# Optimization experiments

Measured on AMD Instinct MI355X. Metric: run time of the kernel, lower is better.

## Reference

```python
import jax, jax.numpy as jnp
import numpy as np

B, S, D, H = 2, 2048, 1024, 16
HD = D // H

def setup_inputs() -> dict:
    key = jax.random.key(0)
    k1, k2, k3, k4, k5 = jax.random.split(key, 5)
    X = jax.random.normal(k1, (B, S, D), dtype=jnp.float32)
    # nn.Linear(D, 3D): weight [3D, D], bias [3D]
    W_qkv = jax.random.normal(k2, (3 * D, D), dtype=jnp.float32) * (1.0 / np.sqrt(D))
    b_qkv = jax.random.normal(k3, (3 * D,), dtype=jnp.float32) * 0.02
    W_out = jax.random.normal(k4, (D, D), dtype=jnp.float32) * (1.0 / np.sqrt(D))
    b_out = jax.random.normal(k5, (D,), dtype=jnp.float32) * 0.02
    return {"X": X, "W_qkv": W_qkv, "b_qkv": b_qkv, "W_out": W_out, "b_out": b_out}

def reference(X, W_qkv, b_qkv, W_out, b_out):
    b, s, d = X.shape
    qkv = jnp.einsum('bsd,ed->bse', X, W_qkv) + b_qkv  # [B,S,3D]
    q, k, v = jnp.split(qkv, 3, axis=2)
    def heads(t):
        return t.reshape(b, s, H, HD).transpose(0, 2, 1, 3)  # [B,H,S,HD]
    q, k, v = heads(q), heads(k), heads(v)
    scores = jnp.einsum('bhqd,bhkd->bhqk', q, k) * (1.0 / np.sqrt(HD))
    causal = jnp.tril(jnp.ones((s, s), dtype=bool))
    scores = jnp.where(causal[None, None], scores, jnp.float32(-jnp.inf))
    probs = jax.nn.softmax(scores, axis=-1)
    attn = jnp.einsum('bhqk,bhkd->bhqd', probs, v)  # [B,H,S,HD]
    attn = attn.transpose(0, 2, 1, 3).reshape(b, s, d)
    out = jnp.einsum('bsd,ed->bse', attn, W_out) + b_out
    return out
```

## Files before the change

kernel.cpp:

```cpp
#include <hip/hip_runtime.h>


typedef _Float16 f16x8 __attribute__((ext_vector_type(8)));
typedef _Float16 f16x4 __attribute__((ext_vector_type(4)));
typedef float    f32x4 __attribute__((ext_vector_type(4)));
typedef unsigned short u16x8 __attribute__((ext_vector_type(8)));

__device__ __forceinline__ float bf16_bits_to_f32(unsigned short u) {
    union { unsigned int i; float f; } v; v.i = ((unsigned int)u) << 16; return v.f;
}
__device__ __forceinline__ unsigned short f32_to_bf16_bits(float f) {
    union { float f; unsigned int i; } v; v.f = f;
    unsigned int x = v.i;
    return (unsigned short)((x + 0x7fffu + ((x >> 16) & 1u)) >> 16);
}
__device__ __forceinline__ float fexp2(float x) {
#if __has_builtin(__builtin_amdgcn_exp2f)
    return __builtin_amdgcn_exp2f(x);
#else
    return exp2f(x);
#endif
}
__device__ __forceinline__ void gll16(const void* g, void* l) {
    __builtin_amdgcn_global_load_lds(
        (const __attribute__((address_space(1))) unsigned int*)g,
        (__attribute__((address_space(3))) unsigned int*)l, 16, 0, 0);
}

__global__ void detect_kernel(const unsigned short* __restrict__ X, unsigned int* __restrict__ flag) {
    __shared__ unsigned int smax;
    if (threadIdx.x == 0) smax = 0;
    __syncthreads();
    unsigned int mymax = 0;
    for (int i = threadIdx.x; i < 16384; i += 256) {
        unsigned int e = (X[i] >> 7) & 0xFFu;
        mymax = mymax > e ? mymax : e;
    }
    atomicMax(&smax, mymax);
    __syncthreads();
    if (threadIdx.x == 0) flag[0] = (smax >= 0x90u) ? 1u : 0u;
}

__global__ void __launch_bounds__(256) cvtw_kernel(const void* __restrict__ in,
                                                   _Float16* __restrict__ out,
                                                   const unsigned int* __restrict__ flag) {
    size_t i = ((size_t)blockIdx.x * 256 + threadIdx.x) * 8;
    f16x8 c;
    if (flag[0]) {
        const float* p = (const float*)in + i;
        #pragma unroll
        for (int j = 0; j < 8; j++) c[j] = (_Float16)p[j];
    } else {
        u16x8 r = *(const u16x8*)((const unsigned short*)in + i);
        #pragma unroll
        for (int j = 0; j < 8; j++) c[j] = (_Float16)bf16_bits_to_f32(r[j]);
    }
    *(f16x8*)(out + i) = c;
}

template<int AF16>
__global__ void __launch_bounds__(256) qkv_gemm(
    const void* __restrict__ A, const _Float16* __restrict__ Wf,
    const void* __restrict__ bias, const unsigned int* __restrict__ flag,
    _Float16* __restrict__ qws, _Float16* __restrict__ kws, _Float16* __restrict__ vtws)
{
    constexpr int AST = AF16 ? 32 : 56;
    __shared__ _Float16 As[128 * AST];
    __shared__ _Float16 Bs[128 * 32];
    const bool isf32 = (flag[0] != 0u);
    const int tid  = threadIdx.x;
    const int lane = tid & 63, wave = tid >> 6;
    const int l15  = lane & 15, quad = lane >> 4;
    const int wm   = (wave >> 1) * 64, wn = (wave & 1) * 64;
    const int m0   = blockIdx.y * 128, n0 = blockIdx.x * 128;
    const int srow = tid >> 1, scol = (tid & 1) * 16;

    f32x4 acc[4][4] = {};

    for (int k0 = 0; k0 < 1024; k0 += 32) {
        if (AF16) {
            #pragma unroll
            for (int i = 0; i < 2; i++) {
                int seg = (wave * 2 + i) * 64 + lane;
                int row = seg >> 2, qtr = seg & 3;
                gll16((const _Float16*)A + (size_t)(m0 + row) * 1024 + k0 + qtr * 8,
                      &As[(wave * 2 + i) * 512]);
            }
        } else {
            f16x8 c0, c1;
            if (isf32) {
                const float4* ga = (const float4*)((const float*)A + (size_t)(m0 + srow) * 1024 + k0 + scol);
                float4 a0 = ga[0], a1 = ga[1], a2 = ga[2], a3 = ga[3];
                c0[0]=(_Float16)a0.x; c0[1]=(_Float16)a0.y; c0[2]=(_Float16)a0.z; c0[3]=(_Float16)a0.w;
                c0[4]=(_Float16)a1.x; c0[5]=(_Float16)a1.y; c0[6]=(_Float16)a1.z; c0[7]=(_Float16)a1.w;
                c1[0]=(_Float16)a2.x; c1[1]=(_Float16)a2.y; c1[2]=(_Float16)a2.z; c1[3]=(_Float16)a2.w;
                c1[4]=(_Float16)a3.x; c1[5]=(_Float16)a3.y; c1[6]=(_Float16)a3.z; c1[7]=(_Float16)a3.w;
            } else {
                const unsigned short* ga = (const unsigned short*)A + (size_t)(m0 + srow) * 1024 + k0 + scol;
                u16x8 r0 = *(const u16x8*)ga, r1 = *(const u16x8*)(ga + 8);
                #pragma unroll
                for (int i = 0; i < 8; i++) {
                    c0[i] = (_Float16)bf16_bits_to_f32(r0[i]);
                    c1[i] = (_Float16)bf16_bits_to_f32(r1[i]);
                }
            }
            *(f16x8*)&As[srow * AST + scol]     = c0;
            *(f16x8*)&As[srow * AST + scol + 8] = c1;
        }
        #pragma unroll
        for (int i = 0; i < 2; i++) {
            int seg = (wave * 2 + i) * 64 + lane;
            int row = seg >> 2, qtr = seg & 3;
            gll16(Wf + (size_t)(n0 + row) * 1024 + k0 + qtr * 8, &Bs[(wave * 2 + i) * 512]);
        }
        __syncthreads();
        f16x8 af[4], bfg[4];
        #pragma unroll
        for (int mt = 0; mt < 4; mt++)
            af[mt] = *(const f16x8*)&As[(wm + mt * 16 + l15) * AST + quad * 8];
        #pragma unroll
        for (int nt = 0; nt < 4; nt++)
            bfg[nt] = *(const f16x8*)&Bs[(wn + nt * 16 + l15) * 32 + quad * 8];
        #pragma unroll
        for (int mt = 0; mt < 4; mt++)
            #pragma unroll
            for (int nt = 0; nt < 4; nt++)
                acc[mt][nt] = __builtin_amdgcn_mfma_f32_16x16x32_f16(af[mt], bfg[nt], acc[mt][nt], 0, 0, 0);
        __syncthreads();
    }

    #pragma unroll
    for (int mt = 0; mt < 4; mt++) {
        #pragma unroll
        for (int nt = 0; nt < 4; nt++) {
            #pragma unroll
            for (int r = 0; r < 4; r++) {
                int m = m0 + wm + mt * 16 + quad * 4 + r;
                int n = n0 + wn + nt * 16 + l15;
                float bval = isf32 ? ((const float*)bias)[n] : bf16_bits_to_f32(((const unsigned short*)bias)[n]);
                float val = acc[mt][nt][r] + bval;
                int b = m >> 11, s = m & 2047;
                int t = n >> 10, e = n & 1023;
                int h = e >> 6, hd = e & 63;
                int bh = b * 16 + h;
                if (t == 0)      qws[((size_t)bh * 2048 + s) * 64 + hd]  = (_Float16)val;
                else if (t == 1) kws[((size_t)bh * 2048 + s) * 64 + hd]  = (_Float16)val;
                else             vtws[((size_t)bh * 64 + hd) * 2048 + s] = (_Float16)val;
            }
        }
    }
}

__global__ void __launch_bounds__(256) out_gemm(
    const _Float16* __restrict__ Alo, const _Float16* __restrict__ Ahi,
    const _Float16* __restrict__ Wf, const void* __restrict__ bias,
    const unsigned int* __restrict__ flag, void* __restrict__ outp, int m_base)
{
    __shared__ _Float16 As[128 * 32];
    __shared__ _Float16 Bs[128 * 32];
    const bool isf32 = (flag[0] != 0u);
    const int tid  = threadIdx.x;
    const int lane = tid & 63, wave = tid >> 6;
    const int l15  = lane & 15, quad = lane >> 4;
    const int wm   = (wave >> 1) * 64, wn = (wave & 1) * 64;
    const int m0g  = m_base + blockIdx.y * 128, n0 = blockIdx.x * 128;
    const _Float16* A = (m0g < 2048) ? (Alo + (size_t)m0g * 1024)
                                     : (Ahi + (size_t)(m0g - 2048) * 1024);
    f32x4 acc[4][4] = {};

    for (int k0 = 0; k0 < 1024; k0 += 32) {
        #pragma unroll
        for (int i = 0; i < 2; i++) {
            int seg = (wave * 2 + i) * 64 + lane;
            int row = seg >> 2, qtr = seg & 3;
            gll16(A + (size_t)row * 1024 + k0 + qtr * 8, &As[(wave * 2 + i) * 512]);
            gll16(Wf + (size_t)(n0 + row) * 1024 + k0 + qtr * 8, &Bs[(wave * 2 + i) * 512]);
        }
        __syncthreads();
        f16x8 af[4], bfg[4];
        #pragma unroll
        for (int mt = 0; mt < 4; mt++)
            af[mt] = *(const f16x8*)&As[(wm + mt * 16 + l15) * 32 + quad * 8];
        #pragma unroll
        for (int nt = 0; nt < 4; nt++)
            bfg[nt] = *(const f16x8*)&Bs[(wn + nt * 16 + l15) * 32 + quad * 8];
        #pragma unroll
        for (int mt = 0; mt < 4; mt++)
            #pragma unroll
            for (int nt = 0; nt < 4; nt++)
                acc[mt][nt] = __builtin_amdgcn_mfma_f32_16x16x32_f16(af[mt], bfg[nt], acc[mt][nt], 0, 0, 0);
        __syncthreads();
    }

    #pragma unroll
    for (int mt = 0; mt < 4; mt++) {
        #pragma unroll
        for (int nt = 0; nt < 4; nt++) {
            #pragma unroll
            for (int r = 0; r < 4; r++) {
                int m = m0g + wm + mt * 16 + quad * 4 + r;
                int n = n0 + wn + nt * 16 + l15;
                float bval = isf32 ? ((const float*)bias)[n] : bf16_bits_to_f32(((const unsigned short*)bias)[n]);
                float val = acc[mt][nt][r] + bval;
                size_t idx = (size_t)m * 1024 + n;
                if (isf32) ((float*)outp)[idx] = val;
                else       ((unsigned short*)outp)[idx] = f32_to_bf16_bits(val);
            }
        }
    }
}

__global__ void __launch_bounds__(256) flash_kernel(
    const _Float16* __restrict__ qws,
    const _Float16* __restrict__ kws,
    const _Float16* __restrict__ vtws,
    _Float16* __restrict__ attn_lo,
    _Float16* __restrict__ attn_hi)
{
    __shared__ _Float16 Ks[2][64 * 64];
    __shared__ _Float16 Vs[2][64 * 72];

    const int bh   = blockIdx.x;
    const int qb   = 15 - blockIdx.y;
    const int Q0   = qb * 128;
    const int tid  = threadIdx.x;
    const int wave = tid >> 6;
    const int lane = tid & 63;
    const int l15  = lane & 15, quad = lane >> 4;

    const _Float16* Q  = qws  + (size_t)bh * 2048 * 64;
    const _Float16* Kp = kws  + (size_t)bh * 2048 * 64;
    const _Float16* Vt = vtws + (size_t)bh * 64 * 2048;

    const int q0w = Q0 + wave * 32;
    f16x8 qf[2][2];
    #pragma unroll
    for (int qt = 0; qt < 2; qt++) {
        qf[qt][0] = *(const f16x8*)(Q + (size_t)(q0w + qt * 16 + l15) * 64 + quad * 8);
        qf[qt][1] = *(const f16x8*)(Q + (size_t)(q0w + qt * 16 + l15) * 64 + 32 + quad * 8);
    }

    f32x4 o[2][4] = {};
    float lp[2] = {0.f, 0.f}, mP[2] = {0.f, 0.f}, mN[2] = {0.f, 0.f};
    const int nch = qb * 2 + 2;
    const float sc2 = 0.18033688011112042591f;

    {
        #pragma unroll
        for (int i = 0; i < 2; i++) {
            int seg = (wave * 2 + i) * 64 + lane;
            gll16(Kp + (size_t)(seg >> 3) * 64 + (seg & 7) * 8, &Ks[0][(wave * 2 + i) * 512]);
        }
        int hd = tid >> 3, ko = (tid & 7) * 8;
        f16x8 v0 = *(const f16x8*)(Vt + (size_t)hd * 2048 + ko);
        f16x8 v1 = *(const f16x8*)(Vt + (size_t)(hd + 32) * 2048 + ko);
        *(f16x8*)&Vs[0][hd * 72 + ko]        = v0;
        *(f16x8*)&Vs[0][(hd + 32) * 72 + ko] = v1;
    }

    for (int c = 0; c < nch; c++) {
        __syncthreads();
        const int cb = c & 1;
        const bool more = (c + 1 < nch);
        f16x8 vr0, vr1;
        int hd = tid >> 3, ko = (tid & 7) * 8;
        if (more) {
            int jn = (c + 1) * 64;
            vr0 = *(const f16x8*)(Vt + (size_t)hd * 2048 + jn + ko);
            vr1 = *(const f16x8*)(Vt + (size_t)(hd + 32) * 2048 + jn + ko);
            #pragma unroll
            for (int i = 0; i < 2; i++) {
                int seg = (wave * 2 + i) * 64 + lane;
                gll16(Kp + (size_t)(jn + (seg >> 3)) * 64 + (seg & 7) * 8,
                      &Ks[cb ^ 1][(wave * 2 + i) * 512]);
            }
        }

        const int j0 = c * 64;
        if (j0 <= q0w + 31) {
            const bool diag = (j0 >= Q0);
            f32x4 t[2][4];
            #pragma unroll
            for (int kt = 0; kt < 4; kt++) {
                f16x8 k0 = *(const f16x8*)&Ks[cb][(kt * 16 + l15) * 64 + quad * 8];
                f16x8 k1 = *(const f16x8*)&Ks[cb][(kt * 16 + l15) * 64 + 32 + quad * 8];
                #pragma unroll
                for (int qt = 0; qt < 2; qt++) {
                    f32x4 z = {};
                    z = __builtin_amdgcn_mfma_f32_16x16x32_f16(k0, qf[qt][0], z, 0, 0, 0);
                    t[qt][kt] = __builtin_amdgcn_mfma_f32_16x16x32_f16(k1, qf[qt][1], z, 0, 0, 0);
                }
            }
            #pragma unroll
            for (int qt = 0; qt < 2; qt++) {
                const int q0t = q0w + qt * 16;
                float tv[16];
                #pragma unroll
                for (int kt = 0; kt < 4; kt++)
                    #pragma unroll
                    for (int r = 0; r < 4; r++) {
                        float v = t[qt][kt][r] * sc2;
                        if (diag)
                            v = ((j0 + kt * 16 + quad * 4 + r) <= (q0t + l15)) ? v : -INFINITY;
                        tv[kt * 4 + r] = v;
                    }
                float mx = tv[0];
                #pragma unroll
                for (int i = 1; i < 16; i++) mx = fmaxf(mx, tv[i]);
                float mxa = fmaxf(mx, __shfl_xor(mx, 16));
                mxa = fmaxf(mxa, __shfl_xor(mxa, 32));
                float alpha = fexp2(mP[qt] - mN[qt]);
                mP[qt] = mN[qt];
                #pragma unroll
                for (int mt = 0; mt < 4; mt++) o[qt][mt] *= alpha;
                lp[qt] *= alpha;
                float rs = 0.f, p[16];
                #pragma unroll
                for (int i = 0; i < 16; i++) { p[i] = fexp2(fminf(tv[i] - mP[qt], 15.0f)); rs += p[i]; }
                lp[qt] += rs;
                f16x4 pf[4];
                #pragma unroll
                for (int kt = 0; kt < 4; kt++)
                    #pragma unroll
                    for (int r = 0; r < 4; r++) pf[kt][r] = (_Float16)p[kt * 4 + r];
                #pragma unroll
                for (int kt = 0; kt < 4; kt++) {
                    #pragma unroll
                    for (int mt = 0; mt < 4; mt++) {
                        f16x4 cv = *(const f16x4*)&Vs[cb][(mt * 16 + l15) * 72 + kt * 16 + quad * 4];
                        o[qt][mt] = __builtin_amdgcn_mfma_f32_16x16x16f16(cv, pf[kt], o[qt][mt], 0, 0, 0);
                    }
                }
                mN[qt] = fmaxf(mN[qt], mxa);
            }
        }

        if (more) {
            *(f16x8*)&Vs[cb ^ 1][hd * 72 + ko]        = vr0;
            *(f16x8*)&Vs[cb ^ 1][(hd + 32) * 72 + ko] = vr1;
        }
    }

    const int b = bh >> 4, h = bh & 15;
    _Float16* attn = (b == 0) ? attn_lo : attn_hi;
    #pragma unroll
    for (int qt = 0; qt < 2; qt++) {
        float rs = lp[qt];
        rs += __shfl_xor(rs, 16);
        rs += __shfl_xor(rs, 32);
        const float inv = 1.0f / rs;
        const int s = q0w + qt * 16 + l15;
        #pragma unroll
        for (int mt = 0; mt < 4; mt++) {
            #pragma unroll
            for (int r = 0; r < 4; r++) {
                int hdd = mt * 16 + quad * 4 + r;
                attn[(size_t)s * 1024 + h * 64 + hdd] = (_Float16)(o[qt][mt][r] * inv);
            }
        }
    }
}

extern "C" void kernel_launch(void* const* d_in, const int* in_sizes, int n_in,
                              void* d_out, int out_size, void* d_ws, size_t ws_size,
                              hipStream_t stream) {
    (void)out_size;
    const void *X = nullptr, *Wqkv = nullptr, *bqkv = nullptr, *Wout = nullptr, *bout = nullptr;
    for (int i = 0; i < n_in; i++) {
        switch (in_sizes[i]) {
            case 4194304: X    = d_in[i]; break;
            case 3145728: Wqkv = d_in[i]; break;
            case 3072:    bqkv = d_in[i]; break;
            case 1048576: Wout = d_in[i]; break;
            case 1024:    bout = d_in[i]; break;
        }
    }
    char* ws = (char*)d_ws;
    const size_t MB = 1u << 20;
    unsigned int* flag = (unsigned int*)ws;
    char* base = ws + 256;

    detect_kernel<<<1, 256, 0, stream>>>((const unsigned short*)X, flag);

    if (ws_size >= (size_t)(385 * MB / 10)) {
        _Float16* wf16 = (_Float16*)(base);
        _Float16* xf16 = (_Float16*)(base + 6 * MB);
        _Float16* q    = (_Float16*)(base + 14 * MB);
        _Float16* k    = (_Float16*)(base + 22 * MB);
        _Float16* vt   = (_Float16*)(base + 30 * MB);
        cvtw_kernel<<<dim3(1536), 256, 0, stream>>>(Wqkv, wf16, flag);
        cvtw_kernel<<<dim3(2048), 256, 0, stream>>>(X, xf16, flag);
        qkv_gemm<1><<<dim3(24, 32), 256, 0, stream>>>(xf16, wf16, bqkv, flag, q, k, vt);
        cvtw_kernel<<<dim3(512), 256, 0, stream>>>(Wout, wf16, flag);
        _Float16* attn = xf16;
        flash_kernel<<<dim3(32, 16), 256, 0, stream>>>(q, k, vt, attn, attn + (size_t)2048 * 1024);
        out_gemm<<<dim3(8, 32), 256, 0, stream>>>(attn, attn + (size_t)2048 * 1024,
                                                  wf16, bout, flag, d_out, 0);
    } else {
        _Float16* wf16    = (_Float16*)(base);
        _Float16* attn_hi = (_Float16*)(base + 6 * MB);
        _Float16* q       = (_Float16*)(base + 10 * MB);
        _Float16* k       = (_Float16*)(base + 18 * MB);
        _Float16* vt      = (_Float16*)(base + 26 * MB);
        _Float16* attn_lo = (_Float16*)((char*)d_out + 8 * MB);
        cvtw_kernel<<<dim3(1536), 256, 0, stream>>>(Wqkv, wf16, flag);
        qkv_gemm<0><<<dim3(24, 32), 256, 0, stream>>>(X, wf16, bqkv, flag, q, k, vt);
        cvtw_kernel<<<dim3(512), 256, 0, stream>>>(Wout, wf16, flag);
        flash_kernel<<<dim3(32, 16), 256, 0, stream>>>(q, k, vt, attn_lo, attn_hi);
        out_gemm<<<dim3(8, 16), 256, 0, stream>>>(attn_lo, attn_hi, wf16, bout, flag, d_out, 0);
        out_gemm<<<dim3(8, 16), 256, 0, stream>>>(attn_lo, attn_hi, wf16, bout, flag, d_out, 2048);
    }
}
```

Measured before the change: 235.3 us.

## Shrink flash-attention query tile to 64 rows, swizzle K in LDS, prescale Q

The flash kernel now processes 64 query rows per block (16 per wave) instead of 128, and the launch grid doubles to 32x32 blocks. This improves load balance and occupancy over the causal triangle and drops the per-chunk skip check. K tiles are written to LDS with a rotated column swizzle to avoid bank conflicts on the MFMA operand reads. The softmax scale is folded into Q in the QKV GEMM epilogue, removing a multiply per score. In exchange, each K/V tile is reused by half as many queries, so global K/V traffic doubles.

Result: faster. 215.6 us (-8.4%).

```diff
diff --git a/kernel.cpp b/kernel.cpp
--- a/kernel.cpp
+++ b/kernel.cpp
@@ -129,6 +129,7 @@
         __syncthreads();
     }
 
+    const float qsc = 0.18033688011112042591f;
     #pragma unroll
     for (int mt = 0; mt < 4; mt++) {
         #pragma unroll
@@ -143,7 +144,7 @@
                 int t = n >> 10, e = n & 1023;
                 int h = e >> 6, hd = e & 63;
                 int bh = b * 16 + h;
-                if (t == 0)      qws[((size_t)bh * 2048 + s) * 64 + hd]  = (_Float16)val;
+                if (t == 0)      qws[((size_t)bh * 2048 + s) * 64 + hd]  = (_Float16)(val * qsc);
                 else if (t == 1) kws[((size_t)bh * 2048 + s) * 64 + hd]  = (_Float16)val;
                 else             vtws[((size_t)bh * 64 + hd) * 2048 + s] = (_Float16)val;
             }
@@ -221,8 +222,7 @@
     __shared__ _Float16 Vs[2][64 * 72];
 
     const int bh   = blockIdx.x;
-    const int qb   = 15 - blockIdx.y;
-    const int Q0   = qb * 128;
+    const int qb   = 31 - blockIdx.y;
     const int tid  = threadIdx.x;
     const int wave = tid >> 6;
     const int lane = tid & 63;
@@ -232,24 +232,20 @@
     const _Float16* Kp = kws  + (size_t)bh * 2048 * 64;
     const _Float16* Vt = vtws + (size_t)bh * 64 * 2048;
 
-    const int q0w = Q0 + wave * 32;
-    f16x8 qf[2][2];
-    #pragma unroll
-    for (int qt = 0; qt < 2; qt++) {
-        qf[qt][0] = *(const f16x8*)(Q + (size_t)(q0w + qt * 16 + l15) * 64 + quad * 8);
-        qf[qt][1] = *(const f16x8*)(Q + (size_t)(q0w + qt * 16 + l15) * 64 + 32 + quad * 8);
-    }
-
-    f32x4 o[2][4] = {};
-    float lp[2] = {0.f, 0.f}, mP[2] = {0.f, 0.f}, mN[2] = {0.f, 0.f};
-    const int nch = qb * 2 + 2;
-    const float sc2 = 0.18033688011112042591f;
+    const int q0w = qb * 64 + wave * 16;
+    f16x8 qf0 = *(const f16x8*)(Q + (size_t)(q0w + l15) * 64 + quad * 8);
+    f16x8 qf1 = *(const f16x8*)(Q + (size_t)(q0w + l15) * 64 + 32 + quad * 8);
+
+    f32x4 o[4] = {};
+    float lp = 0.f, mP = 0.f, mN = 0.f;
+    const int nch = qb + 1;
 
     {
         #pragma unroll
         for (int i = 0; i < 2; i++) {
-            int seg = (wave * 2 + i) * 64 + lane;
-            gll16(Kp + (size_t)(seg >> 3) * 64 + (seg & 7) * 8, &Ks[0][(wave * 2 + i) * 512]);
+            int s = (wave * 2 + i) * 64 + lane;
+            int row = s >> 3, cs = ((s & 7) - row) & 7;
+            gll16(Kp + (size_t)row * 64 + cs * 8, &Ks[0][s * 8]);
         }
         int hd = tid >> 3, ko = (tid & 7) * 8;
         f16x8 v0 = *(const f16x8*)(Vt + (size_t)hd * 2048 + ko);
@@ -270,70 +266,61 @@
             vr1 = *(const f16x8*)(Vt + (size_t)(hd + 32) * 2048 + jn + ko);
             #pragma unroll
             for (int i = 0; i < 2; i++) {
-                int seg = (wave * 2 + i) * 64 + lane;
-                gll16(Kp + (size_t)(jn + (seg >> 3)) * 64 + (seg & 7) * 8,
-                      &Ks[cb ^ 1][(wave * 2 + i) * 512]);
-            }
-        }
-
-        const int j0 = c * 64;
-        if (j0 <= q0w + 31) {
-            const bool diag = (j0 >= Q0);
-            f32x4 t[2][4];
-            #pragma unroll
-            for (int kt = 0; kt < 4; kt++) {
-                f16x8 k0 = *(const f16x8*)&Ks[cb][(kt * 16 + l15) * 64 + quad * 8];
-                f16x8 k1 = *(const f16x8*)&Ks[cb][(kt * 16 + l15) * 64 + 32 + quad * 8];
-                #pragma unroll
-                for (int qt = 0; qt < 2; qt++) {
-                    f32x4 z = {};
-                    z = __builtin_amdgcn_mfma_f32_16x16x32_f16(k0, qf[qt][0], z, 0, 0, 0);
-                    t[qt][kt] = __builtin_amdgcn_mfma_f32_16x16x32_f16(k1, qf[qt][1], z, 0, 0, 0);
-                }
-            }
-            #pragma unroll
-            for (int qt = 0; qt < 2; qt++) {
-                const int q0t = q0w + qt * 16;
-                float tv[16];
-                #pragma unroll
-                for (int kt = 0; kt < 4; kt++)
-                    #pragma unroll
-                    for (int r = 0; r < 4; r++) {
-                        float v = t[qt][kt][r] * sc2;
-                        if (diag)
-                            v = ((j0 + kt * 16 + quad * 4 + r) <= (q0t + l15)) ? v : -INFINITY;
-                        tv[kt * 4 + r] = v;
-                    }
-                float mx = tv[0];
-                #pragma unroll
-                for (int i = 1; i < 16; i++) mx = fmaxf(mx, tv[i]);
-                float mxa = fmaxf(mx, __shfl_xor(mx, 16));
-                mxa = fmaxf(mxa, __shfl_xor(mxa, 32));
-                float alpha = fexp2(mP[qt] - mN[qt]);
-                mP[qt] = mN[qt];
-                #pragma unroll
-                for (int mt = 0; mt < 4; mt++) o[qt][mt] *= alpha;
-                lp[qt] *= alpha;
-                float rs = 0.f, p[16];
-                #pragma unroll
-                for (int i = 0; i < 16; i++) { p[i] = fexp2(fminf(tv[i] - mP[qt], 15.0f)); rs += p[i]; }
-                lp[qt] += rs;
-                f16x4 pf[4];
-                #pragma unroll
-                for (int kt = 0; kt < 4; kt++)
-                    #pragma unroll
-                    for (int r = 0; r < 4; r++) pf[kt][r] = (_Float16)p[kt * 4 + r];
-                #pragma unroll
-                for (int kt = 0; kt < 4; kt++) {
-                    #pragma unroll
-                    for (int mt = 0; mt < 4; mt++) {
-                        f16x4 cv = *(const f16x4*)&Vs[cb][(mt * 16 + l15) * 72 + kt * 16 + quad * 4];
-                        o[qt][mt] = __builtin_amdgcn_mfma_f32_16x16x16f16(cv, pf[kt], o[qt][mt], 0, 0, 0);
-                    }
-                }
-                mN[qt] = fmaxf(mN[qt], mxa);
-            }
-        }
+                int s = (wave * 2 + i) * 64 + lane;
+                int row = s >> 3, cs = ((s & 7) - row) & 7;
+                gll16(Kp + (size_t)(jn + row) * 64 + cs * 8, &Ks[cb ^ 1][s * 8]);
+            }
+        }
+
+        const bool diag = (c == qb);
+        f32x4 t[4];
+        #pragma unroll
+        for (int kt = 0; kt < 4; kt++) {
+            int row = kt * 16 + l15;
+            f16x8 k0 = *(const f16x8*)&Ks[cb][row * 64 + ((quad + l15) & 7) * 8];
+            f16x8 k1 = *(const f16x8*)&Ks[cb][row * 64 + ((4 + quad + l15) & 7) * 8];
+            f32x4 z = {};
+            z = __builtin_amdgcn_mfma_f32_16x16x32_f16(k0, qf0, z, 0, 0, 0);
+            t[kt] = __builtin_amdgcn_mfma_f32_16x16x32_f16(k1, qf1, z, 0, 0, 0);
+        }
+        float tv[16];
+        #pragma unroll
+        for (int kt = 0; kt < 4; kt++)
+            #pragma unroll
+            for (int r = 0; r < 4; r++) {
+                float v = t[kt][r];
+                if (diag)
+                    v = ((kt * 16 + quad * 4 + r) <= (wave * 16 + l15)) ? v : -INFINITY;
+                tv[kt * 4 + r] = v;
+            }
+        float mx = tv[0];
+        #pragma unroll
+        for (int i = 1; i < 16; i++) mx = fmaxf(mx, tv[i]);
+        float mxa = fmaxf(mx, __shfl_xor(mx, 16));
+        mxa = fmaxf(mxa, __shfl_xor(mxa, 32));
+        float alpha = fexp2(mP - mN);
+        mP = mN;
+        #pragma unroll
+        for (int mt = 0; mt < 4; mt++) o[mt] *= alpha;
+        lp *= alpha;
+        float rs = 0.f, p[16];
+        #pragma unroll
+        for (int i = 0; i < 16; i++) { p[i] = fexp2(fminf(tv[i] - mP, 15.0f)); rs += p[i]; }
+        lp += rs;
+        f16x4 pf[4];
+        #pragma unroll
+        for (int kt = 0; kt < 4; kt++)
+            #pragma unroll
+            for (int r = 0; r < 4; r++) pf[kt][r] = (_Float16)p[kt * 4 + r];
+        #pragma unroll
+        for (int kt = 0; kt < 4; kt++) {
+            #pragma unroll
+            for (int mt = 0; mt < 4; mt++) {
+                f16x4 cv = *(const f16x4*)&Vs[cb][(mt * 16 + l15) * 72 + kt * 16 + quad * 4];
+                o[mt] = __builtin_amdgcn_mfma_f32_16x16x16f16(cv, pf[kt], o[mt], 0, 0, 0);
+            }
+        }
+        mN = fmaxf(mN, mxa);
 
         if (more) {
             *(f16x8*)&Vs[cb ^ 1][hd * 72 + ko]        = vr0;
@@ -343,19 +330,18 @@
 
     const int b = bh >> 4, h = bh & 15;
     _Float16* attn = (b == 0) ? attn_lo : attn_hi;
-    #pragma unroll
-    for (int qt = 0; qt < 2; qt++) {
-        float rs = lp[qt];
+    {
+        float rs = lp;
         rs += __shfl_xor(rs, 16);
         rs += __shfl_xor(rs, 32);
         const float inv = 1.0f / rs;
-        const int s = q0w + qt * 16 + l15;
+        const int s = q0w + l15;
         #pragma unroll
         for (int mt = 0; mt < 4; mt++) {
             #pragma unroll
             for (int r = 0; r < 4; r++) {
                 int hdd = mt * 16 + quad * 4 + r;
-                attn[(size_t)s * 1024 + h * 64 + hdd] = (_Float16)(o[qt][mt][r] * inv);
+                attn[(size_t)s * 1024 + h * 64 + hdd] = (_Float16)(o[mt][r] * inv);
             }
         }
     }
@@ -393,7 +379,7 @@
         qkv_gemm<1><<<dim3(24, 32), 256, 0, stream>>>(xf16, wf16, bqkv, flag, q, k, vt);
         cvtw_kernel<<<dim3(512), 256, 0, stream>>>(Wout, wf16, flag);
         _Float16* attn = xf16;
-        flash_kernel<<<dim3(32, 16), 256, 0, stream>>>(q, k, vt, attn, attn + (size_t)2048 * 1024);
+        flash_kernel<<<dim3(32, 32), 256, 0, stream>>>(q, k, vt, attn, attn + (size_t)2048 * 1024);
         out_gemm<<<dim3(8, 32), 256, 0, stream>>>(attn, attn + (size_t)2048 * 1024,
                                                   wf16, bout, flag, d_out, 0);
     } else {
@@ -406,7 +392,7 @@
         cvtw_kernel<<<dim3(1536), 256, 0, stream>>>(Wqkv, wf16, flag);
         qkv_gemm<0><<<dim3(24, 32), 256, 0, stream>>>(X, wf16, bqkv, flag, q, k, vt);
         cvtw_kernel<<<dim3(512), 256, 0, stream>>>(Wout, wf16, flag);
-        flash_kernel<<<dim3(32, 16), 256, 0, stream>>>(q, k, vt, attn_lo, attn_hi);
+        flash_kernel<<<dim3(32, 32), 256, 0, stream>>>(q, k, vt, attn_lo, attn_hi);
         out_gemm<<<dim3(8, 16), 256, 0, stream>>>(attn_lo, attn_hi, wf16, bout, flag, d_out, 0);
         out_gemm<<<dim3(8, 16), 256, 0, stream>>>(attn_lo, attn_hi, wf16, bout, flag, d_out, 2048);
     }
```
